# Kernel optimization log

Measured on AMD Instinct MI355X. Metric: run time of the kernel, lower is better.

## Reference

```python
import jax, jax.numpy as jnp
import numpy as np

B, C, Hs, Ws = 8, 512, 32, 32
NUM_HEADS, D_K = 8, 64
SCALE = D_K ** -0.5


def setup_inputs() -> dict:
    key = jax.random.key(0)
    ks = jax.random.split(key, 8)
    inner = NUM_HEADS * D_K  # 512
    s = 0.02
    return {
        "x": jax.random.normal(ks[0], (B, C, Hs, Ws), dtype=jnp.float32),
        "y": jax.random.normal(ks[1], (B, C, Hs, Ws), dtype=jnp.float32),
        "Wq": jax.random.normal(ks[2], (inner, C), dtype=jnp.float32) * s,
        "bq": jnp.zeros((inner,), dtype=jnp.float32),
        "Wkv": jax.random.normal(ks[3], (2 * inner, C), dtype=jnp.float32) * s,
        "bkv": jnp.zeros((2 * inner,), dtype=jnp.float32),
        "Wp": jax.random.normal(ks[4], (C, inner), dtype=jnp.float32) * s,
        "bp": jnp.zeros((C,), dtype=jnp.float32),
    }


def reference(x, y, Wq, bq, Wkv, bkv, Wp, bp):
    # Faithful to CrossAttentionBlock.forward: y is only shape-checked, unused.
    x_shape = x.shape
    b, c = x.shape[0], x.shape[1]
    # channel_transfer: [B, C, H, W] -> [B, H, W, C] -> [B, N, C]
    xt = jnp.transpose(x, (0, 2, 3, 1)).reshape(b, -1, c)
    n = xt.shape[1]
    # q: [B, N, H*dk] -> [B, H, N, dk]
    q = (xt @ Wq.T + bq).reshape(b, n, NUM_HEADS, D_K).transpose(0, 2, 1, 3)
    # kv: [B, N, 2*H*dk] -> [2, B, H, N, dk]
    kv = (xt @ Wkv.T + bkv).reshape(b, n, 2, NUM_HEADS, D_K).transpose(2, 0, 3, 1, 4)
    k, v = kv[0], kv[1]
    atten = jnp.einsum("bhik,bhjk->bhij", q, k) * SCALE
    atten = jax.nn.softmax(atten, axis=-1)
    res = jnp.einsum("bhij,bhjd->bhid", atten, v)  # [B, H, N, dk]
    res = res.transpose(0, 2, 1, 3).reshape(b, n, NUM_HEADS * D_K)
    res = res @ Wp.T + bp  # [B, N, C]
    # original does a raw reshape of [B, N, C] back into x_shape [B, C, H, W]
    return res.reshape(x_shape)
```

## Files before the change

### kernel.cpp

```cpp
#include <hip/hip_runtime.h>
#include <math.h>

#define BB 8
#define CC 512
#define NH 8
#define DK 64
#define NN 1024
#define MROWS (BB * NN)
#define INNER 512
#define SCALE 0.125f

typedef __attribute__((ext_vector_type(8))) short bf16x8;
typedef __attribute__((ext_vector_type(4))) float floatx4;

__device__ inline short f2bf(float f) {
    union { float f; unsigned u; } un;
    un.f = f;
    unsigned r = un.u + 0x7fffu + ((un.u >> 16) & 1u);
    return (short)(r >> 16);
}

__device__ inline short f2bf_rhu(float f) {
    union { float f; unsigned u; } un;
    un.f = f;
    return (short)((un.u + 0x8000u) >> 16);
}

#define GLD_LDS(gptr, lptr)                                                  \
    __builtin_amdgcn_global_load_lds(                                        \
        (const __attribute__((address_space(1))) void*)(gptr),               \
        (__attribute__((address_space(3))) void*)(lptr), 16, 0, 0)

__global__ __launch_bounds__(256) void prep_kernel(
    const float* __restrict__ x, const float* __restrict__ Wq,
    const float* __restrict__ Wkv, const float* __restrict__ Wp,
    const float* __restrict__ bq, const float* __restrict__ bkv,
    short* __restrict__ xtb, short* __restrict__ wqkvb,
    short* __restrict__ wpb, float* __restrict__ bqkv) {
    __shared__ float tile[32][33];
    const int bid = blockIdx.x;
    if (bid < 4096) {
        const int n0 = (bid & 31) * 32;
        const int c0 = ((bid >> 5) & 15) * 32;
        const int b = bid >> 9;
        const int tx = threadIdx.x & 31;
        const int ty = threadIdx.x >> 5;
        const float* xb = x + (size_t)b * CC * NN;
        short* xo = xtb + (size_t)b * NN * CC;
        for (int i = ty; i < 32; i += 8)
            tile[i][tx] = xb[(size_t)(c0 + i) * NN + n0 + tx];
        __syncthreads();
        for (int i = ty; i < 32; i += 8)
            xo[(size_t)(n0 + i) * CC + c0 + tx] = f2bf(tile[tx][i]);
    } else {
        const int i = (bid - 4096) * 1024 + threadIdx.x * 4;
        if (i < 786432) {
            float4 v = (i < 262144) ? *(const float4*)&Wq[i]
                                    : *(const float4*)&Wkv[i - 262144];
            wqkvb[i + 0] = f2bf(v.x);
            wqkvb[i + 1] = f2bf(v.y);
            wqkvb[i + 2] = f2bf(v.z);
            wqkvb[i + 3] = f2bf(v.w);
        } else if (i < 1048576) {
            const int j = i - 786432;
            float4 v = *(const float4*)&Wp[j];
            wpb[j + 0] = f2bf(v.x);
            wpb[j + 1] = f2bf(v.y);
            wpb[j + 2] = f2bf(v.z);
            wpb[j + 3] = f2bf(v.w);
        } else {
            const int j = i - 1048576;
            if (j < 1536) {
                float4 v = (j < 512) ? *(const float4*)&bq[j]
                                     : *(const float4*)&bkv[j - 512];
                *(float4*)&bqkv[j] = v;
            }
        }
    }
}

template <int MODE, int BN>
__global__ __launch_bounds__(256) void gemm_mfma_kernel(
    const short* __restrict__ A, const short* __restrict__ W,
    const float* __restrict__ bias, float* __restrict__ outf,
    short* __restrict__ outq, short* __restrict__ outk,
    short* __restrict__ outv) {
    constexpr int K = 512;
    constexpr int WCOLS = BN / 64;
    constexpr int WROWS = 4 / WCOLS;
    constexpr int WRSPAN = 128 / WROWS;
    constexpr int RT = WRSPAN / 16;
    __shared__ short As[128 * 32];
    __shared__ short Bs[BN * 32];

    const int t = threadIdx.x;
    const int wave = t >> 6;
    const int lane = t & 63;
    const int col = lane & 15;
    const int quad = lane >> 4;
    const int wr = wave / WCOLS;
    const int wc = wave % WCOLS;

    const int bm0 = blockIdx.y * 128;
    const int bn0 = blockIdx.x * BN;

    floatx4 acc[RT][4];
#pragma unroll
    for (int i = 0; i < RT; i++)
#pragma unroll
        for (int j = 0; j < 4; j++) acc[i][j] = (floatx4){0.f, 0.f, 0.f, 0.f};

    const int kpE = (lane & 3) * 8;
    const int rA = wave * 32 + (lane >> 2);
    const short* Ag = A + (size_t)(bm0 + rA) * K + kpE;
    short* AsW = As + wave * 1024;
    const int rB = wave * (BN / 4) + (lane >> 2);
    const short* Wg = W + (size_t)(bn0 + rB) * K + kpE;
    short* BsW = Bs + wave * (BN / 4) * 32;

    for (int k0 = 0; k0 < K; k0 += 32) {
        __syncthreads();
        GLD_LDS(Ag + k0, AsW);
        GLD_LDS(Ag + 16 * K + k0, AsW + 512);
        if constexpr (BN == 128) {
            GLD_LDS(Wg + k0, BsW);
            GLD_LDS(Wg + 16 * K + k0, BsW + 512);
        } else {
            GLD_LDS(Wg + k0, BsW);
        }
        __syncthreads();

        bf16x8 aF[RT], bF[4];
#pragma unroll
        for (int rt = 0; rt < RT; rt++)
            aF[rt] =
                *(const bf16x8*)&As[(wr * WRSPAN + rt * 16 + col) * 32 + quad * 8];
#pragma unroll
        for (int ct = 0; ct < 4; ct++)
            bF[ct] = *(const bf16x8*)&Bs[(wc * 64 + ct * 16 + col) * 32 + quad * 8];
#pragma unroll
        for (int rt = 0; rt < RT; rt++)
#pragma unroll
            for (int ct = 0; ct < 4; ct++)
                acc[rt][ct] = __builtin_amdgcn_mfma_f32_16x16x32_bf16(
                    aF[rt], bF[ct], acc[rt][ct], 0, 0, 0);
    }

#pragma unroll
    for (int rt = 0; rt < RT; rt++) {
#pragma unroll
        for (int ct = 0; ct < 4; ct++) {
            const int jn = bn0 + wc * 64 + ct * 16 + col;
            const float bsv = bias[jn];
#pragma unroll
            for (int r = 0; r < 4; r++) {
                const int m = bm0 + wr * WRSPAN + rt * 16 + quad * 4 + r;
                const float val = acc[rt][ct][r] + bsv;
                if (MODE == 0) {
                    outf[(size_t)m * 512 + jn] = val;
                } else {
                    const int b = m >> 10;
                    const int n = m & 1023;
                    const int reg = jn >> 9;
                    const int h = (jn >> 6) & 7;
                    const int d = jn & 63;
                    if (reg == 0)
                        outq[(((size_t)(b * NH + h)) * NN + n) * DK + d] =
                            f2bf(val * SCALE);
                    else if (reg == 1)
                        outk[(((size_t)(b * NH + h)) * NN + n) * DK + d] = f2bf(val);
                    else
                        outv[(((size_t)(b * NH + h)) * DK + d) * NN + n] = f2bf(val);
                }
            }
        }
    }
}

__global__ __launch_bounds__(512) void attn_mfma_kernel(
    const short* __restrict__ q, const short* __restrict__ k,
    const short* __restrict__ vt, short* __restrict__ out) {
    const int bh = blockIdx.y;
    const int b = bh >> 3;
    const int h = bh & 7;
    const int n0 = blockIdx.x * 128;
    const int tid = threadIdx.x;
    const int wave = tid >> 6;
    const int lane = tid & 63;
    const int col = lane & 15;
    const int quad = lane >> 4;

    __shared__ short Ks[2][64 * 64];
    __shared__ short Vs[2][64 * 64];
    __shared__ short Ps[8][16][72];

    bf16x8 qa0, qa1;
    {
        const size_t qoff = ((size_t)bh * NN + n0 + wave * 16 + col) * DK;
        qa0 = *(const bf16x8*)&q[qoff + quad * 8];
        qa1 = *(const bf16x8*)&q[qoff + 32 + quad * 8];
    }

    floatx4 o[4];
#pragma unroll
    for (int i = 0; i < 4; i++) o[i] = (floatx4){0.f, 0.f, 0.f, 0.f};
    float l_run[4] = {0.f, 0.f, 0.f, 0.f};

    const short* kg = k + (size_t)bh * NN * DK;
    const short* vg = vt + (size_t)bh * DK * NN;

    const int srow = lane >> 3;
    const int sunit = (lane & 7) ^ srow;
    const int sbase = (wave & 3) * 16;

    const int xs = col & 7;
    const int pK0 = (quad ^ xs) * 8;
    const int pK1 = ((quad + 4) ^ xs) * 8;

#define STAGE(J0, BUF)                                                         \
    do {                                                                       \
        if (wave < 4) {                                                        \
            GLD_LDS(kg + (size_t)((J0) + sbase + srow) * DK + sunit * 8,       \
                    &Ks[BUF][sbase * 64]);                                     \
            GLD_LDS(kg + (size_t)((J0) + sbase + 8 + srow) * DK + sunit * 8,   \
                    &Ks[BUF][(sbase + 8) * 64]);                               \
        } else {                                                               \
            GLD_LDS(vg + (size_t)(sbase + srow) * NN + (J0) + sunit * 8,       \
                    &Vs[BUF][sbase * 64]);                                     \
            GLD_LDS(vg + (size_t)(sbase + 8 + srow) * NN + (J0) + sunit * 8,   \
                    &Vs[BUF][(sbase + 8) * 64]);                               \
        }                                                                      \
    } while (0)

    STAGE(0, 0);

    for (int c = 0; c < 16; c++) {
        const int buf = c & 1;
        __syncthreads();
        if (c < 15) STAGE((c + 1) * 64, buf ^ 1);

        const short* K_ = &Ks[buf][0];
        const short* V_ = &Vs[buf][0];

        float p[4][4];
#pragma unroll
        for (int ct = 0; ct < 4; ct++) {
            bf16x8 kb0 = *(const bf16x8*)&K_[(ct * 16 + col) * 64 + pK0];
            bf16x8 kb1 = *(const bf16x8*)&K_[(ct * 16 + col) * 64 + pK1];
            floatx4 acc = (floatx4){0.f, 0.f, 0.f, 0.f};
            acc = __builtin_amdgcn_mfma_f32_16x16x32_bf16(qa0, kb0, acc, 0, 0, 0);
            acc = __builtin_amdgcn_mfma_f32_16x16x32_bf16(qa1, kb1, acc, 0, 0, 0);
#pragma unroll
            for (int r = 0; r < 4; r++) p[ct][r] = __expf(acc[r]);
        }

#pragma unroll
        for (int r = 0; r < 4; r++)
            l_run[r] += (p[0][r] + p[1][r]) + (p[2][r] + p[3][r]);

#pragma unroll
        for (int ct = 0; ct < 4; ct++)
#pragma unroll
            for (int r = 0; r < 4; r++)
                Ps[wave][quad * 4 + r][ct * 16 + col] = f2bf_rhu(p[ct][r]);

        bf16x8 pa0 = *(const bf16x8*)&Ps[wave][col][quad * 8];
        bf16x8 pa1 = *(const bf16x8*)&Ps[wave][col][32 + quad * 8];

#pragma unroll
        for (int dt = 0; dt < 4; dt++) {
            bf16x8 vb0 = *(const bf16x8*)&V_[(dt * 16 + col) * 64 + pK0];
            bf16x8 vb1 = *(const bf16x8*)&V_[(dt * 16 + col) * 64 + pK1];
            o[dt] = __builtin_amdgcn_mfma_f32_16x16x32_bf16(pa0, vb0, o[dt], 0, 0, 0);
            o[dt] = __builtin_amdgcn_mfma_f32_16x16x32_bf16(pa1, vb1, o[dt], 0, 0, 0);
        }
    }
#undef STAGE

#pragma unroll
    for (int r = 0; r < 4; r++) {
        float lv = l_run[r];
#pragma unroll
        for (int d = 1; d < 16; d <<= 1) lv += __shfl_xor(lv, d, 64);
        const float inv = 1.f / lv;
        const int m = n0 + wave * 16 + quad * 4 + r;
        short* orow = out + ((size_t)(b * NN + m)) * 512 + h * 64;
#pragma unroll
        for (int dt = 0; dt < 4; dt++) orow[dt * 16 + col] = f2bf(o[dt][r] * inv);
    }
}

extern "C" void kernel_launch(void* const* d_in, const int* in_sizes, int n_in,
                              void* d_out, int out_size, void* d_ws,
                              size_t ws_size, hipStream_t stream) {
    const float* x = (const float*)d_in[0];
    const float* Wq = (const float*)d_in[2];
    const float* bq = (const float*)d_in[3];
    const float* Wkv = (const float*)d_in[4];
    const float* bkv = (const float*)d_in[5];
    const float* Wp = (const float*)d_in[6];
    const float* bp = (const float*)d_in[7];
    float* out = (float*)d_out;

    short* ws = (short*)d_ws;
    short* xtb = ws;
    short* qb = xtb + (size_t)MROWS * CC;
    short* kb = qb + (size_t)MROWS * INNER;
    short* vb = kb + (size_t)MROWS * INNER;
    short* wqkvb = vb + (size_t)MROWS * INNER;
    short* wpb = wqkvb + (size_t)3 * INNER * CC;
    float* bqkv = (float*)(wpb + (size_t)CC * INNER);
    short* att = xtb;

    prep_kernel<<<4096 + 1026, 256, 0, stream>>>(x, Wq, Wkv, Wp, bq, bkv, xtb,
                                                 wqkvb, wpb, bqkv);
    {
        dim3 grid((3 * INNER) / 128, MROWS / 128);
        gemm_mfma_kernel<1, 128><<<grid, 256, 0, stream>>>(
            xtb, wqkvb, bqkv, nullptr, qb, kb, vb);
    }
    {
        dim3 grid(NN / 128, BB * NH);
        attn_mfma_kernel<<<grid, 512, 0, stream>>>(qb, kb, vb, att);
    }
    {
        dim3 grid(CC / 64, MROWS / 128);
        gemm_mfma_kernel<0, 64><<<grid, 256, 0, stream>>>(
            att, wpb, bp, out, nullptr, nullptr, nullptr);
    }
}
```

Before: 161.6 us.

## Double-buffer GEMM LDS tiles and swap grid dimensions for block ordering

The GEMM kernel now uses two LDS buffers and issues the global-to-LDS loads for the next K-step before computing on the current one, removing one barrier per iteration. This is meant to hide global load latency behind the MFMA work. Separately, the grid axes of both GEMMs and the attention kernel are swapped so that consecutive blocks walk the M or head dimension first, which changes which blocks share cached weights and K/V in L2. LDS use doubles, which may lower occupancy, and dropping the trailing barrier depends on the load having completed before the next iteration's sync.

```diff
diff --git a/kernel.cpp b/kernel.cpp
--- a/kernel.cpp
+++ b/kernel.cpp
@@ -90,8 +90,10 @@
     constexpr int WROWS = 4 / WCOLS;
     constexpr int WRSPAN = 128 / WROWS;
     constexpr int RT = WRSPAN / 16;
-    __shared__ short As[128 * 32];
-    __shared__ short Bs[BN * 32];
+    constexpr int ABUF = 128 * 32;
+    constexpr int BBUF = BN * 32;
+    __shared__ short As[2 * ABUF];
+    __shared__ short Bs[2 * BBUF];
 
     const int t = threadIdx.x;
     const int wave = t >> 6;
@@ -101,8 +103,8 @@
     const int wr = wave / WCOLS;
     const int wc = wave % WCOLS;
 
-    const int bm0 = blockIdx.y * 128;
-    const int bn0 = blockIdx.x * BN;
+    const int bm0 = blockIdx.x * 128;
+    const int bn0 = blockIdx.y * BN;
 
     floatx4 acc[RT][4];
 #pragma unroll
@@ -113,31 +115,41 @@
     const int kpE = (lane & 3) * 8;
     const int rA = wave * 32 + (lane >> 2);
     const short* Ag = A + (size_t)(bm0 + rA) * K + kpE;
-    short* AsW = As + wave * 1024;
     const int rB = wave * (BN / 4) + (lane >> 2);
     const short* Wg = W + (size_t)(bn0 + rB) * K + kpE;
-    short* BsW = Bs + wave * (BN / 4) * 32;
-
-    for (int k0 = 0; k0 < K; k0 += 32) {
+    const int aOff = wave * 1024;
+    const int bOff = wave * (BN / 4) * 32;
+
+#define GSTAGE(K0, BUF)                                                       \
+    do {                                                                      \
+        GLD_LDS(Ag + (K0), As + (BUF)*ABUF + aOff);                           \
+        GLD_LDS(Ag + 16 * K + (K0), As + (BUF)*ABUF + aOff + 512);            \
+        if constexpr (BN == 128) {                                            \
+            GLD_LDS(Wg + (K0), Bs + (BUF)*BBUF + bOff);                       \
+            GLD_LDS(Wg + 16 * K + (K0), Bs + (BUF)*BBUF + bOff + 512);        \
+        } else {                                                              \
+            GLD_LDS(Wg + (K0), Bs + (BUF)*BBUF + bOff);                       \
+        }                                                                     \
+    } while (0)
+
+    GSTAGE(0, 0);
+
+#pragma unroll
+    for (int it = 0; it < 16; it++) {
+        const int buf = it & 1;
         __syncthreads();
-        GLD_LDS(Ag + k0, AsW);
-        GLD_LDS(Ag + 16 * K + k0, AsW + 512);
-        if constexpr (BN == 128) {
-            GLD_LDS(Wg + k0, BsW);
-            GLD_LDS(Wg + 16 * K + k0, BsW + 512);
-        } else {
-            GLD_LDS(Wg + k0, BsW);
-        }
-        __syncthreads();
-
+        if (it < 15) GSTAGE((it + 1) * 32, buf ^ 1);
+
+        const short* A_ = As + buf * ABUF;
+        const short* B_ = Bs + buf * BBUF;
         bf16x8 aF[RT], bF[4];
 #pragma unroll
         for (int rt = 0; rt < RT; rt++)
             aF[rt] =
-                *(const bf16x8*)&As[(wr * WRSPAN + rt * 16 + col) * 32 + quad * 8];
+                *(const bf16x8*)&A_[(wr * WRSPAN + rt * 16 + col) * 32 + quad * 8];
 #pragma unroll
         for (int ct = 0; ct < 4; ct++)
-            bF[ct] = *(const bf16x8*)&Bs[(wc * 64 + ct * 16 + col) * 32 + quad * 8];
+            bF[ct] = *(const bf16x8*)&B_[(wc * 64 + ct * 16 + col) * 32 + quad * 8];
 #pragma unroll
         for (int rt = 0; rt < RT; rt++)
 #pragma unroll
@@ -145,6 +157,7 @@
                 acc[rt][ct] = __builtin_amdgcn_mfma_f32_16x16x32_bf16(
                     aF[rt], bF[ct], acc[rt][ct], 0, 0, 0);
     }
+#undef GSTAGE
 
 #pragma unroll
     for (int rt = 0; rt < RT; rt++) {
@@ -180,10 +193,10 @@
 __global__ __launch_bounds__(512) void attn_mfma_kernel(
     const short* __restrict__ q, const short* __restrict__ k,
     const short* __restrict__ vt, short* __restrict__ out) {
-    const int bh = blockIdx.y;
+    const int bh = blockIdx.x;
     const int b = bh >> 3;
     const int h = bh & 7;
-    const int n0 = blockIdx.x * 128;
+    const int n0 = blockIdx.y * 128;
     const int tid = threadIdx.x;
     const int wave = tid >> 6;
     const int lane = tid & 63;
@@ -315,16 +328,16 @@
     prep_kernel<<<4096 + 1026, 256, 0, stream>>>(x, Wq, Wkv, Wp, bq, bkv, xtb,
                                                  wqkvb, wpb, bqkv);
     {
-        dim3 grid((3 * INNER) / 128, MROWS / 128);
+        dim3 grid(MROWS / 128, (3 * INNER) / 128);
         gemm_mfma_kernel<1, 128><<<grid, 256, 0, stream>>>(
             xtb, wqkvb, bqkv, nullptr, qb, kb, vb);
     }
     {
-        dim3 grid(NN / 128, BB * NH);
+        dim3 grid(BB * NH, NN / 128);
         attn_mfma_kernel<<<grid, 512, 0, stream>>>(qb, kb, vb, att);
     }
     {
-        dim3 grid(CC / 64, MROWS / 128);
+        dim3 grid(MROWS / 128, CC / 64);
         gemm_mfma_kernel<0, 64><<<grid, 256, 0, stream>>>(
             att, wpb, bp, out, nullptr, nullptr, nullptr);
     }
```

Measured after the change: 161.6 us. No clear change (-0.0%).
